# Kernel optimization log

Hardware: AMD Instinct MI355X
Metric: run time of the kernel (lower is better)

The kernel has to match this reference:

```python
import jax, jax.numpy as jnp
import numpy as np

B, C, H, W = 128, 1280, 16, 16


def _conv1x1(x, w, b):
    # 1x1 conv == per-pixel linear over channels: (O,C) x (B,C,H,W) -> (B,O,H,W)
    return jnp.einsum('oc,bchw->bohw', w, x) + b[None, :, None, None]


def setup_inputs() -> dict:
    key = jax.random.key(0)
    ks = jax.random.split(key, 10)
    s = 1.0 / np.sqrt(C)
    inp = {
        'x': jax.random.normal(ks[0], (B, C, H, W), dtype=jnp.float32),
        'Wk': jax.random.uniform(ks[1], (C, C), jnp.float32, -s, s),
        'bk': jax.random.uniform(ks[2], (C,), jnp.float32, -s, s),
        'Wq': jax.random.uniform(ks[3], (C, C), jnp.float32, -s, s),
        'bq': jax.random.uniform(ks[4], (C,), jnp.float32, -s, s),
        'Wv': jax.random.uniform(ks[5], (C, C), jnp.float32, -s, s),
        'bv': jax.random.uniform(ks[6], (C,), jnp.float32, -s, s),
        'Wr': jax.random.uniform(ks[7], (C, C), jnp.float32, -s, s),
        'br': jax.random.uniform(ks[8], (C,), jnp.float32, -s, s),
        'alpha': 0.1 * jax.random.normal(ks[9], (1,), dtype=jnp.float32),
    }
    return inp


def reference(x, Wk, bk, Wq, bq, Wv, bv, Wr, br, alpha):
    b, c, h, w = x.shape
    hw = h * w
    k = _conv1x1(x, Wk, bk).reshape(b, c, hw)   # (B,C,HW)
    q = _conv1x1(x, Wq, bq).reshape(b, c, hw)   # (B,C,HW)
    v = _conv1x1(x, Wv, bv).reshape(b, c, hw)   # (B,C,HW)
    # K^T Q: (B,HW,HW) == keys.view.permute(0,2,1) @ queries.view
    scores = jnp.einsum('bcn,bcm->bnm', k, q)
    # torch.nn.Softmax2d on a 3D tensor applies softmax over dim=-3 (here: batch)
    attn = jax.nn.softmax(scores, axis=0)
    # attn @ V^T: (B,HW,HW) @ (B,HW,C) -> (B,HW,C)
    att = jnp.einsum('bnm,bmc->bnc', attn, v.transpose(0, 2, 1))
    att = att.transpose(0, 2, 1).reshape(b, c, h, w)
    out = _conv1x1(att, Wr, br)
    return alpha * out + x
```

## Files before the change

### kernel.cpp

```cpp
#include <hip/hip_runtime.h>
#include <hip/hip_bf16.h>

typedef __attribute__((ext_vector_type(8))) short bf16x8;
typedef __attribute__((ext_vector_type(4))) float f32x4;

#define GLD16(g, s) __builtin_amdgcn_global_load_lds( \
    (const __attribute__((address_space(1))) void*)(g), \
    (__attribute__((address_space(3))) void*)(s), 16, 0, 0)

#define SBAR() __builtin_amdgcn_sched_barrier(0)
#define WAIT_LGKM(n) do { asm volatile("s_waitcnt lgkmcnt(" #n ")" ::: "memory"); SBAR(); } while (0)

static constexpr int kB  = 128;
static constexpr int kC  = 1280;
static constexpr int kHW = 256;

__device__ __forceinline__ float bf2f(unsigned short u) {
    return __uint_as_float(((unsigned int)u) << 16);
}

template<int OUT_MODE, int BIAS_MODE, int ORDER>
__global__ __launch_bounds__(512, 2) void gemm_q(
    const __hip_bfloat16* __restrict__ A,
    const __hip_bfloat16* __restrict__ Bt,
    void* __restrict__ outp,
    const float* __restrict__ bias,
    const float* __restrict__ resid,
    const float* __restrict__ alphap,
    const float* __restrict__ aux1,
    const float* __restrict__ aux2,
    int M, int N, int K,
    int ldA, int ldB, long sA, long sB, long sC, int ldC)
{
    extern __shared__ char smem[];
    const int t = threadIdx.x;
    const int w = t >> 6, l = t & 63;
    const int q = l >> 4, r16 = l & 15;
    const int wr = w >> 2, wc = w & 3;
    const int z = blockIdx.z;
    const int nbm = M >> 8, nbn = N >> 8;
    const int nwg = nbm * nbn;
    int f = blockIdx.x;
    {
        const int q8 = nwg >> 3, r8 = nwg & 7;
        const int xcd = f & 7, rank = f >> 3;
        f = (xcd < r8 ? xcd * (q8 + 1) : r8 * (q8 + 1) + (xcd - r8) * q8) + rank;
    }
    long m0, n0;
    if (ORDER == 0) { m0 = (long)(f % nbm) << 8; n0 = (long)(f / nbm) << 8; }
    else            { n0 = (long)(f % nbn) << 8; m0 = (long)(f / nbn) << 8; }
    const char* Azb = (const char*)(A + (long)z * sA);
    const char* Bzb = (const char*)(Bt + (long)z * sB);

    const char* pa[4];
    const char* pb[4];
    int ldsd[4];
    #pragma unroll
    for (int i = 0; i < 4; ++i) {
        const int d = i * 8192 + t * 16;
        const int row = d >> 7;
        const int cb = (d & 127) ^ ((row & 7) << 4);
        pa[i] = Azb + ((m0 + row) * (long)ldA) * 2 + cb;
        pb[i] = Bzb + ((n0 + row) * (long)ldB) * 2 + cb;
        ldsd[i] = d;
    }
    auto stage = [&](int slot) {
        char* base = smem + slot * 65536;
        #pragma unroll
        for (int i = 0; i < 4; ++i) GLD16(pa[i], base + ldsd[i]);
        #pragma unroll
        for (int i = 0; i < 4; ++i) GLD16(pb[i], base + 32768 + ldsd[i]);
        #pragma unroll
        for (int i = 0; i < 4; ++i) { pa[i] += 128; pb[i] += 128; }
    };

    const int mask = (l & 7) << 4;
    const int s0 = ((l >> 5) << 4) ^ mask;
    (void)s0;
    const int cx  = (q << 4) ^ mask;
    int offA[2], offB[2];
    offA[0] = (wr * 128 + r16) * 128 + cx;
    offA[1] = (wr * 128 + r16) * 128 + (cx ^ 64);
    offB[0] = 32768 + (wc * 64 + r16) * 128 + cx;
    offB[1] = 32768 + (wc * 64 + r16) * 128 + (cx ^ 64);

#define DSA(dst, bs_, mih, kk) do { const char* p_ = (bs_) + offA[kk] + (mih) * 8192; \
    dst[0] = *(const bf16x8*)(p_);        dst[1] = *(const bf16x8*)(p_ + 2048); \
    dst[2] = *(const bf16x8*)(p_ + 4096); dst[3] = *(const bf16x8*)(p_ + 6144); } while (0)
#define DSB(dst, bs_, kk) do { const char* p_ = (bs_) + offB[kk]; \
    dst[0] = *(const bf16x8*)(p_);        dst[1] = *(const bf16x8*)(p_ + 2048); \
    dst[2] = *(const bf16x8*)(p_ + 4096); dst[3] = *(const bf16x8*)(p_ + 6144); } while (0)
#define MM16(ar, br, mih) do { __builtin_amdgcn_s_setprio(1); \
    _Pragma("unroll") for (int j = 0; j < 4; ++j) \
    _Pragma("unroll") for (int ni = 0; ni < 4; ++ni) \
        acc[(mih) * 4 + j][ni] = __builtin_amdgcn_mfma_f32_16x16x32_bf16( \
            ar[j], br[ni], acc[(mih) * 4 + j][ni], 0, 0, 0); \
    __builtin_amdgcn_s_setprio(0); SBAR(); } while (0)

    f32x4 acc[8][4] = {};
    const int nK = K >> 6;
    stage(0);

    for (int tk = 0; tk < nK; ++tk) {
        const int s = tk & 1;
        asm volatile("s_waitcnt vmcnt(0)" ::: "memory");
        SBAR();
        __builtin_amdgcn_s_barrier();
        SBAR();
        if (tk + 1 < nK) stage(s ^ 1);
        SBAR();

        const char* bs_ = smem + s * 65536;
        bf16x8 aP[4], bP[4], aQ[4], bQ[4];
        DSB(bP, bs_, 0); DSA(aP, bs_, 0, 0);
        DSA(aQ, bs_, 1, 0);
        WAIT_LGKM(4);  MM16(aP, bP, 0);
        DSB(bQ, bs_, 1); DSA(aP, bs_, 0, 1);
        WAIT_LGKM(8);  MM16(aQ, bP, 1);
        DSA(aQ, bs_, 1, 1);
        WAIT_LGKM(4);  MM16(aP, bQ, 0);
        WAIT_LGKM(0);  MM16(aQ, bQ, 1);
        asm volatile("s_waitcnt lgkmcnt(0)" ::: "memory");
        SBAR();
        __builtin_amdgcn_s_barrier();
        SBAR();
    }

    const float alpha = (OUT_MODE >= 3) ? alphap[0] : 0.0f;
    #pragma unroll
    for (int mi = 0; mi < 8; ++mi) {
        #pragma unroll
        for (int ni = 0; ni < 4; ++ni) {
            #pragma unroll
            for (int r = 0; r < 4; ++r) {
                const long row = m0 + wr * 128 + mi * 16 + q * 4 + r;
                const long col = n0 + wc * 64 + ni * 16 + r16;
                float vv = acc[mi][ni][r];
                if (BIAS_MODE == 1) vv += bias[col];
                if (BIAS_MODE == 2) vv += bias[row];
                if (OUT_MODE == 0) {
                    ((__hip_bfloat16*)outp)[(long)z * sC + row * ldC + col] = __float2bfloat16(vv);
                } else if (OUT_MODE == 1) {
                    ((float*)outp)[(long)z * sC + row * ldC + col] = vv;
                } else if (OUT_MODE == 2) {
                    const long addr = (col >> 8) * (long)(kC * kHW) + row * kHW + (col & 255);
                    ((__hip_bfloat16*)outp)[addr] = __float2bfloat16(vv);
                } else if (OUT_MODE == 3) {
                    const long addr = (col >> 8) * (long)(kC * kHW) + row * kHW + (col & 255);
                    ((float*)outp)[addr] = alpha * vv + resid[addr];
                } else {
                    const long addr = (long)z * (kC * kHW) + row * kHW + col;
                    const float term = vv + aux1[row] * aux2[(long)z * 256 + col] + bias[row];
                    ((float*)outp)[addr] = alpha * term + resid[addr];
                }
            }
        }
    }
#undef DSA
#undef DSB
#undef MM16
}

__global__ __launch_bounds__(256) void transpose_x(
    const float* __restrict__ x, __hip_bfloat16* __restrict__ xT)
{
    __shared__ float tile[64][65];
    const int b = blockIdx.z;
    const int c0 = blockIdx.x * 64;
    const int p0 = blockIdx.y * 64;
    const int tj = threadIdx.x & 63;
    const int ti = threadIdx.x >> 6;
    const float* xb = x + ((long)b * kC + c0) * kHW + p0;
    #pragma unroll
    for (int i = 0; i < 16; ++i) {
        const int c = i * 4 + ti;
        tile[c][tj] = xb[(long)c * kHW + tj];
    }
    __syncthreads();
    __hip_bfloat16* o = xT + ((long)(b * kHW + p0)) * kC + c0;
    #pragma unroll
    for (int i = 0; i < 16; ++i) {
        const int p = i * 4 + ti;
        o[(long)p * kC + tj] = __float2bfloat16(tile[tj][p]);
    }
}

__global__ __launch_bounds__(256) void transpose_w(
    const float* __restrict__ W, __hip_bfloat16* __restrict__ WT)
{
    __shared__ float tile[64][65];
    const int o0 = blockIdx.x * 64;
    const int c0 = blockIdx.y * 64;
    const int tj = threadIdx.x & 63;
    const int ti = threadIdx.x >> 6;
    #pragma unroll
    for (int i = 0; i < 16; ++i) {
        const int o = i * 4 + ti;
        tile[o][tj] = W[(long)(o0 + o) * kC + c0 + tj];
    }
    __syncthreads();
    #pragma unroll
    for (int i = 0; i < 16; ++i) {
        const int c = i * 4 + ti;
        WT[(long)(c0 + c) * kC + o0 + tj] = __float2bfloat16(tile[tj][c]);
    }
}

__global__ __launch_bounds__(256) void convert_f32_bf16(
    const float* __restrict__ s, __hip_bfloat16* __restrict__ d)
{
    const int i = (blockIdx.x * 256 + threadIdx.x) * 4;
    const float4 f = *reinterpret_cast<const float4*>(s + i);
    d[i + 0] = __float2bfloat16(f.x);
    d[i + 1] = __float2bfloat16(f.y);
    d[i + 2] = __float2bfloat16(f.z);
    d[i + 3] = __float2bfloat16(f.w);
}

__global__ __launch_bounds__(256) void gemv_col(
    const float* __restrict__ Wk, const float* __restrict__ bq,
    const float* __restrict__ Wq, const float* __restrict__ bk,
    float* __restrict__ w1, float* __restrict__ w2)
{
    const float* W = blockIdx.y ? Wq : Wk;
    const float* v = blockIdx.y ? bk : bq;
    float* out = blockIdx.y ? w2 : w1;
    const int lj = threadIdx.x & 63;
    const int wid = threadIdx.x >> 6;
    const int c = blockIdx.x * 64 + lj;
    __shared__ float red[4][64];
    float s = 0.0f;
    for (int o = wid * 320; o < (wid + 1) * 320; ++o)
        s += W[(long)o * kC + c] * v[o];
    red[wid][lj] = s;
    __syncthreads();
    if (wid == 0) out[c] = red[0][lj] + red[1][lj] + red[2][lj] + red[3][lj];
}

__global__ __launch_bounds__(256) void gemv_row(
    const float* __restrict__ Wr, const float* __restrict__ bv, float* __restrict__ out)
{
    const int wid = threadIdx.x >> 6, lj = threadIdx.x & 63;
    const int o = blockIdx.x * 4 + wid;
    float s = 0.0f;
    #pragma unroll
    for (int j = 0; j < 20; ++j)
        s += Wr[(long)o * kC + j * 64 + lj] * bv[j * 64 + lj];
    #pragma unroll
    for (int off = 32; off > 0; off >>= 1) s += __shfl_down(s, off);
    if (lj == 0) out[o] = s;
}

__global__ __launch_bounds__(256) void dot_k(
    const float* __restrict__ a, const float* __restrict__ b, float* __restrict__ out)
{
    __shared__ float red[256];
    const int t_ = threadIdx.x;
    float s = 0.0f;
    for (int j = t_; j < kC; j += 256) s += a[j] * b[j];
    red[t_] = s; __syncthreads();
    for (int off = 128; off > 0; off >>= 1) {
        if (t_ < off) red[t_] += red[t_ + off];
        __syncthreads();
    }
    if (t_ == 0) out[0] = red[0];
}

__global__ __launch_bounds__(256) void row_dot_x(
    const __hip_bfloat16* __restrict__ xT, const float* __restrict__ w2,
    float* __restrict__ c2s)
{
    const int wid = threadIdx.x >> 6, lj = threadIdx.x & 63;
    const long p = (long)blockIdx.x * 4 + wid;
    const ushort4* base = (const ushort4*)((const char*)xT + p * 2560 + lj * 40);
    float s = 0.0f;
    #pragma unroll
    for (int j = 0; j < 5; ++j) {
        const ushort4 v = base[j];
        const int c0 = lj * 20 + j * 4;
        s += bf2f(v.x) * w2[c0] + bf2f(v.y) * w2[c0 + 1]
           + bf2f(v.z) * w2[c0 + 2] + bf2f(v.w) * w2[c0 + 3];
    }
    #pragma unroll
    for (int off = 32; off > 0; off >>= 1) s += __shfl_down(s, off);
    if (lj == 0) c2s[p] = s;
}

__global__ __launch_bounds__(256) void rowsum_attn(
    const __hip_bfloat16* __restrict__ attn, float* __restrict__ rs)
{
    const int wid = threadIdx.x >> 6, lj = threadIdx.x & 63;
    const long p = (long)blockIdx.x * 4 + wid;
    const ushort4 v = *(const ushort4*)((const char*)attn + p * 512 + lj * 8);
    float s = bf2f(v.x) + bf2f(v.y) + bf2f(v.z) + bf2f(v.w);
    #pragma unroll
    for (int off = 32; off > 0; off >>= 1) s += __shfl_down(s, off);
    if (lj == 0) rs[p] = s;
}

__global__ __launch_bounds__(256) void softmax_batch(
    const float* __restrict__ sc, __hip_bfloat16* __restrict__ attn,
    const float* __restrict__ c2s, const float* __restrict__ c0p)
{
    const int pos = blockIdx.x * 256 + threadIdx.x;
    const int mcol = pos & 255;
    const float c0v = c0p[0];
    float m = -3.0e38f, s = 0.0f;
    for (int b = 0; b < kB; ++b) {
        const float v = sc[(long)b * 65536 + pos] + c2s[b * 256 + mcol] + c0v;
        const float mn = fmaxf(m, v);
        s = s * __expf(m - mn) + __expf(v - mn);
        m = mn;
    }
    const float rinv = 1.0f / s;
    for (int b = 0; b < kB; ++b) {
        const float v = sc[(long)b * 65536 + pos] + c2s[b * 256 + mcol] + c0v;
        attn[(long)b * 65536 + pos] = __float2bfloat16(__expf(v - m) * rinv);
    }
}

extern "C" void kernel_launch(void* const* d_in, const int* in_sizes, int n_in,
                              void* d_out, int out_size, void* d_ws, size_t ws_size,
                              hipStream_t stream)
{
    const float* x  = (const float*)d_in[0];
    const float* Wk = (const float*)d_in[1];
    const float* bk = (const float*)d_in[2];
    const float* Wq = (const float*)d_in[3];
    const float* bq = (const float*)d_in[4];
    const float* Wv = (const float*)d_in[5];
    const float* bv = (const float*)d_in[6];
    const float* Wr = (const float*)d_in[7];
    const float* br = (const float*)d_in[8];
    const float* al = (const float*)d_in[9];

    char* ws = (char*)d_ws;
    __hip_bfloat16* xT   = (__hip_bfloat16*)(ws);
    __hip_bfloat16* uT   = (__hip_bfloat16*)(ws + 83886080L);
    __hip_bfloat16* rv   = (__hip_bfloat16*)(ws + 167772160L);
    float*          sc   = (float*)(ws + 251658240L);
    __hip_bfloat16* attn = (__hip_bfloat16*)(ws + 285212672L);
    __hip_bfloat16* WkT  = (__hip_bfloat16*)(ws + 301989888L);
    __hip_bfloat16* Wrb  = (__hip_bfloat16*)(ws + 305266688L);
    __hip_bfloat16* WqT  = (__hip_bfloat16*)(ws + 308543488L);
    __hip_bfloat16* WvT  = (__hip_bfloat16*)(ws + 311820288L);
    __hip_bfloat16* G    = (__hip_bfloat16*)(ws + 315097088L);
    __hip_bfloat16* W2   = (__hip_bfloat16*)(ws + 318373888L);
    float*          w1   = (float*)(ws + 321650688L);
    float*          w2v  = (float*)(ws + 321655808L);
    float*          wrbv = (float*)(ws + 321660928L);
    float*          c0b  = (float*)(ws + 321666048L);
    float*          c2s  = (float*)(ws + 321666560L);
    float*          rs   = (float*)(ws + 321797632L);

    const int SMEM = 131072;
    hipFuncSetAttribute((const void*)gemm_q<0,0,0>, hipFuncAttributeMaxDynamicSharedMemorySize, SMEM);
    hipFuncSetAttribute((const void*)gemm_q<0,1,1>, hipFuncAttributeMaxDynamicSharedMemorySize, SMEM);
    hipFuncSetAttribute((const void*)gemm_q<1,0,0>, hipFuncAttributeMaxDynamicSharedMemorySize, SMEM);
    hipFuncSetAttribute((const void*)gemm_q<2,0,0>, hipFuncAttributeMaxDynamicSharedMemorySize, SMEM);
    hipFuncSetAttribute((const void*)gemm_q<4,0,0>, hipFuncAttributeMaxDynamicSharedMemorySize, SMEM);

    convert_f32_bf16<<<1600, 256, 0, stream>>>(Wr, Wrb);
    transpose_w<<<dim3(20, 20), 256, 0, stream>>>(Wk, WkT);
    transpose_w<<<dim3(20, 20), 256, 0, stream>>>(Wq, WqT);
    transpose_w<<<dim3(20, 20), 256, 0, stream>>>(Wv, WvT);
    gemv_col<<<dim3(20, 2), 256, 0, stream>>>(Wk, bq, Wq, bk, w1, w2v);
    gemv_row<<<320, 256, 0, stream>>>(Wr, bv, wrbv);
    dot_k<<<1, 256, 0, stream>>>(bk, bq, c0b);
    transpose_x<<<dim3(20, 4, 128), 256, 0, stream>>>(x, xT);

    gemm_q<0, 0, 0><<<dim3(25, 1, 2), 512, SMEM, stream>>>(WkT, WqT, G,
        nullptr, nullptr, nullptr, nullptr, nullptr,
        1280, 1280, 1280, 1280, 1280, 1638400, 1638400, 1638400, 1280);
    gemm_q<0, 1, 1><<<dim3(640, 1, 1), 512, SMEM, stream>>>(xT, G, uT,
        w1, nullptr, nullptr, nullptr, nullptr,
        32768, 1280, 1280, 1280, 1280, 0, 0, 0, 1280);
    row_dot_x<<<8192, 256, 0, stream>>>(xT, w2v, c2s);
    gemm_q<1, 0, 0><<<dim3(1, 1, 128), 512, SMEM, stream>>>(xT, uT, sc,
        nullptr, nullptr, nullptr, nullptr, nullptr,
        256, 256, 1280, 1280, 1280, 327680, 327680, 65536, 256);
    softmax_batch<<<256, 256, 0, stream>>>(sc, attn, c2s, c0b);
    rowsum_attn<<<8192, 256, 0, stream>>>(attn, rs);
    gemm_q<2, 0, 0><<<dim3(640, 1, 1), 512, SMEM, stream>>>(W2, xT, rv,
        nullptr, nullptr, nullptr, nullptr, nullptr,
        1280, 32768, 1280, 1280, 1280, 0, 0, 0, 0);
    gemm_q<4, 0, 0><<<dim3(5, 1, 128), 512, SMEM, stream>>>(rv, attn, d_out,
        br, x, al, wrbv, rs,
        1280, 256, 256, 256, 256, 327680, 65536, 0, 0);
}
```

Before: 546.4 us.

## Merge independent GEMMs into one launch and fuse row-dot into transpose

The xT·G GEMM and the W2·xT GEMM are independent, so they now run as a single launch that picks the GEMM from blockIdx.z. This removes a launch and lets the two 640-block grids fill the GPU together. The three weight transposes become one launch, and the c2s row-dot is folded into transpose_x using atomicAdd after an extra zeroing kernel. The atomics add contention and make the summation order nondeterministic. The GEMM body is factored into a forceinline device function so both entry points can share it.

```diff
diff --git a/kernel.cpp b/kernel.cpp
--- a/kernel.cpp
+++ b/kernel.cpp
@@ -20,7 +20,7 @@
 }
 
 template<int OUT_MODE, int BIAS_MODE, int ORDER>
-__global__ __launch_bounds__(512, 2) void gemm_q(
+__device__ __forceinline__ void gemm_body(
     const __hip_bfloat16* __restrict__ A,
     const __hip_bfloat16* __restrict__ Bt,
     void* __restrict__ outp,
@@ -30,14 +30,13 @@
     const float* __restrict__ aux1,
     const float* __restrict__ aux2,
     int M, int N, int K,
-    int ldA, int ldB, long sA, long sB, long sC, int ldC)
-{
-    extern __shared__ char smem[];
+    int ldA, int ldB, long sA, long sB, long sC, int ldC,
+    char* smem, int z)
+{
     const int t = threadIdx.x;
     const int w = t >> 6, l = t & 63;
     const int q = l >> 4, r16 = l & 15;
     const int wr = w >> 2, wc = w & 3;
-    const int z = blockIdx.z;
     const int nbm = M >> 8, nbn = N >> 8;
     const int nwg = nbm * nbn;
     int f = blockIdx.x;
@@ -75,8 +74,6 @@
     };
 
     const int mask = (l & 7) << 4;
-    const int s0 = ((l >> 5) << 4) ^ mask;
-    (void)s0;
     const int cx  = (q << 4) ^ mask;
     int offA[2], offB[2];
     offA[0] = (wr * 128 + r16) * 128 + cx;
@@ -161,10 +158,48 @@
 #undef MM16
 }
 
+template<int OUT_MODE, int BIAS_MODE, int ORDER>
+__global__ __launch_bounds__(512, 2) void gemm_q(
+    const __hip_bfloat16* __restrict__ A,
+    const __hip_bfloat16* __restrict__ Bt,
+    void* __restrict__ outp,
+    const float* __restrict__ bias,
+    const float* __restrict__ resid,
+    const float* __restrict__ alphap,
+    const float* __restrict__ aux1,
+    const float* __restrict__ aux2,
+    int M, int N, int K,
+    int ldA, int ldB, long sA, long sB, long sC, int ldC)
+{
+    extern __shared__ char smem[];
+    gemm_body<OUT_MODE, BIAS_MODE, ORDER>(A, Bt, outp, bias, resid, alphap,
+        aux1, aux2, M, N, K, ldA, ldB, sA, sB, sC, ldC, smem, blockIdx.z);
+}
+
+__global__ __launch_bounds__(512, 2) void gemm_dual(
+    const __hip_bfloat16* __restrict__ xT,
+    const __hip_bfloat16* __restrict__ G,
+    __hip_bfloat16* __restrict__ uT,
+    const float* __restrict__ w1,
+    const __hip_bfloat16* __restrict__ W2,
+    __hip_bfloat16* __restrict__ rv)
+{
+    extern __shared__ char smem[];
+    if (blockIdx.z == 0) {
+        gemm_body<0, 1, 1>(xT, G, uT, w1, nullptr, nullptr, nullptr, nullptr,
+            32768, 1280, 1280, 1280, 1280, 0, 0, 0, 1280, smem, 0);
+    } else {
+        gemm_body<2, 0, 0>(W2, xT, rv, nullptr, nullptr, nullptr, nullptr, nullptr,
+            1280, 32768, 1280, 1280, 1280, 0, 0, 0, 0, smem, 0);
+    }
+}
+
 __global__ __launch_bounds__(256) void transpose_x(
-    const float* __restrict__ x, __hip_bfloat16* __restrict__ xT)
+    const float* __restrict__ x, __hip_bfloat16* __restrict__ xT,
+    const float* __restrict__ w2, float* __restrict__ c2s)
 {
     __shared__ float tile[64][65];
+    __shared__ float red[4][64];
     const int b = blockIdx.z;
     const int c0 = blockIdx.x * 64;
     const int p0 = blockIdx.y * 64;
@@ -183,11 +218,23 @@
         const int p = i * 4 + ti;
         o[(long)p * kC + tj] = __float2bfloat16(tile[tj][p]);
     }
-}
-
-__global__ __launch_bounds__(256) void transpose_w(
-    const float* __restrict__ W, __hip_bfloat16* __restrict__ WT)
-{
+    float s = 0.0f;
+    #pragma unroll
+    for (int j = 0; j < 16; ++j)
+        s += tile[ti * 16 + j][tj] * w2[c0 + ti * 16 + j];
+    red[ti][tj] = s;
+    __syncthreads();
+    if (ti == 0)
+        atomicAdd(&c2s[b * 256 + p0 + tj], red[0][tj] + red[1][tj] + red[2][tj] + red[3][tj]);
+}
+
+__global__ __launch_bounds__(256) void transpose_w3(
+    const float* __restrict__ Wk, __hip_bfloat16* __restrict__ WkT,
+    const float* __restrict__ Wq, __hip_bfloat16* __restrict__ WqT,
+    const float* __restrict__ Wv, __hip_bfloat16* __restrict__ WvT)
+{
+    const float* W = (blockIdx.z == 0) ? Wk : (blockIdx.z == 1) ? Wq : Wv;
+    __hip_bfloat16* WT = (blockIdx.z == 0) ? WkT : (blockIdx.z == 1) ? WqT : WvT;
     __shared__ float tile[64][65];
     const int o0 = blockIdx.x * 64;
     const int c0 = blockIdx.y * 64;
@@ -215,6 +262,12 @@
     d[i + 1] = __float2bfloat16(f.y);
     d[i + 2] = __float2bfloat16(f.z);
     d[i + 3] = __float2bfloat16(f.w);
+}
+
+__global__ __launch_bounds__(256) void zero_f32(float* __restrict__ p)
+{
+    reinterpret_cast<float4*>(p)[blockIdx.x * 256 + threadIdx.x] =
+        make_float4(0.f, 0.f, 0.f, 0.f);
 }
 
 __global__ __launch_bounds__(256) void gemv_col(
@@ -264,26 +317,6 @@
         __syncthreads();
     }
     if (t_ == 0) out[0] = red[0];
-}
-
-__global__ __launch_bounds__(256) void row_dot_x(
-    const __hip_bfloat16* __restrict__ xT, const float* __restrict__ w2,
-    float* __restrict__ c2s)
-{
-    const int wid = threadIdx.x >> 6, lj = threadIdx.x & 63;
-    const long p = (long)blockIdx.x * 4 + wid;
-    const ushort4* base = (const ushort4*)((const char*)xT + p * 2560 + lj * 40);
-    float s = 0.0f;
-    #pragma unroll
-    for (int j = 0; j < 5; ++j) {
-        const ushort4 v = base[j];
-        const int c0 = lj * 20 + j * 4;
-        s += bf2f(v.x) * w2[c0] + bf2f(v.y) * w2[c0 + 1]
-           + bf2f(v.z) * w2[c0 + 2] + bf2f(v.w) * w2[c0 + 3];
-    }
-    #pragma unroll
-    for (int off = 32; off > 0; off >>= 1) s += __shfl_down(s, off);
-    if (lj == 0) c2s[p] = s;
 }
 
 __global__ __launch_bounds__(256) void rowsum_attn(
@@ -355,35 +388,27 @@
 
     const int SMEM = 131072;
     hipFuncSetAttribute((const void*)gemm_q<0,0,0>, hipFuncAttributeMaxDynamicSharedMemorySize, SMEM);
-    hipFuncSetAttribute((const void*)gemm_q<0,1,1>, hipFuncAttributeMaxDynamicSharedMemorySize, SMEM);
     hipFuncSetAttribute((const void*)gemm_q<1,0,0>, hipFuncAttributeMaxDynamicSharedMemorySize, SMEM);
-    hipFuncSetAttribute((const void*)gemm_q<2,0,0>, hipFuncAttributeMaxDynamicSharedMemorySize, SMEM);
     hipFuncSetAttribute((const void*)gemm_q<4,0,0>, hipFuncAttributeMaxDynamicSharedMemorySize, SMEM);
+    hipFuncSetAttribute((const void*)gemm_dual,     hipFuncAttributeMaxDynamicSharedMemorySize, SMEM);
 
     convert_f32_bf16<<<1600, 256, 0, stream>>>(Wr, Wrb);
-    transpose_w<<<dim3(20, 20), 256, 0, stream>>>(Wk, WkT);
-    transpose_w<<<dim3(20, 20), 256, 0, stream>>>(Wq, WqT);
-    transpose_w<<<dim3(20, 20), 256, 0, stream>>>(Wv, WvT);
+    transpose_w3<<<dim3(20, 20, 3), 256, 0, stream>>>(Wk, WkT, Wq, WqT, Wv, WvT);
     gemv_col<<<dim3(20, 2), 256, 0, stream>>>(Wk, bq, Wq, bk, w1, w2v);
     gemv_row<<<320, 256, 0, stream>>>(Wr, bv, wrbv);
     dot_k<<<1, 256, 0, stream>>>(bk, bq, c0b);
-    transpose_x<<<dim3(20, 4, 128), 256, 0, stream>>>(x, xT);
+    zero_f32<<<32, 256, 0, stream>>>(c2s);
+    transpose_x<<<dim3(20, 4, 128), 256, 0, stream>>>(x, xT, w2v, c2s);
 
     gemm_q<0, 0, 0><<<dim3(25, 1, 2), 512, SMEM, stream>>>(WkT, WqT, G,
         nullptr, nullptr, nullptr, nullptr, nullptr,
         1280, 1280, 1280, 1280, 1280, 1638400, 1638400, 1638400, 1280);
-    gemm_q<0, 1, 1><<<dim3(640, 1, 1), 512, SMEM, stream>>>(xT, G, uT,
-        w1, nullptr, nullptr, nullptr, nullptr,
-        32768, 1280, 1280, 1280, 1280, 0, 0, 0, 1280);
-    row_dot_x<<<8192, 256, 0, stream>>>(xT, w2v, c2s);
+    gemm_dual<<<dim3(640, 1, 2), 512, SMEM, stream>>>(xT, G, uT, w1, W2, rv);
     gemm_q<1, 0, 0><<<dim3(1, 1, 128), 512, SMEM, stream>>>(xT, uT, sc,
         nullptr, nullptr, nullptr, nullptr, nullptr,
         256, 256, 1280, 1280, 1280, 327680, 327680, 65536, 256);
     softmax_batch<<<256, 256, 0, stream>>>(sc, attn, c2s, c0b);
     rowsum_attn<<<8192, 256, 0, stream>>>(attn, rs);
-    gemm_q<2, 0, 0><<<dim3(640, 1, 1), 512, SMEM, stream>>>(W2, xT, rv,
-        nullptr, nullptr, nullptr, nullptr, nullptr,
-        1280, 32768, 1280, 1280, 1280, 0, 0, 0, 0);
     gemm_q<4, 0, 0><<<dim3(5, 1, 128), 512, SMEM, stream>>>(rv, attn, d_out,
         br, x, al, wrbv, rs,
         1280, 256, 256, 256, 256, 327680, 65536, 0, 0);
```

New measurement: 509.5 us. 6.7% less time.
